# Kernel optimization log

Hardware: AMD Instinct MI355X
Metric: run time of the kernel (lower is better)

The kernel has to match this reference:

```python
import jax, jax.numpy as jnp
import numpy as np

L = 19          # kernel size (module default l=19, odd -> symmetric reflect pad)
PAD = L // 2    # 9


def _sv_blur(x, kernel):
    """Faithful jax version of BatchBlur_SV spatially-varying branch.

    x:      (B, C, H, W) image, C must be 3 (branch hard-codes expand(3,...))
    kernel: (B, H*W, L, L) per-pixel blur kernels
    """
    B, C, H, W = x.shape
    pad = jnp.pad(x, ((0, 0), (0, 0), (PAD, PAD), (PAD, PAD)), mode='reflect')
    # unfold: (B*C, 1, Hp, Wp) -> (B*C, L*L, H, W); channel dim is the L*L taps
    # in row-major (ki, kj) order, matching torch F.unfold for 1-channel input.
    patches = jax.lax.conv_general_dilated_patches(
        pad.reshape(B * C, 1, H + 2 * PAD, W + 2 * PAD),
        filter_shape=(L, L), window_strides=(1, 1), padding='VALID',
        dimension_numbers=('NCHW', 'OIHW', 'NCHW'))
    # -> (B*C, H*W, L*L), batch-major over (b, c) exactly like pad.view(C*B,...)
    patches = patches.reshape(B * C, L * L, H * W).transpose(0, 2, 1)
    # kernel.flatten(2).unsqueeze(0).expand(3,...).view(-1, HW, L*L):
    # channel-major flatten over (c, b) -- reproduce the original ordering.
    kf = jnp.broadcast_to(kernel.reshape(B, H * W, L * L)[None],
                          (C, B, H * W, L * L)).reshape(C * B, H * W, L * L)
    out = jnp.einsum('npk,npk->np', patches, kf)  # multiply + sum over taps
    return out.reshape(B, C, H, W)


def setup_inputs() -> dict:
    key = jax.random.key(0)
    k1, k2 = jax.random.split(key)
    B, C, H, W = 2, 3, 192, 192
    x = jax.random.normal(k1, (B, C, H, W), dtype=jnp.float32)
    kernel = jax.random.uniform(k2, (B, H * W, L, L), dtype=jnp.float32)
    return {"input": x, "kernel": kernel}


def reference(input, kernel):
    return _sv_blur(input, kernel)
```

## Files before the change

### kernel.cpp

```cpp
#include <hip/hip_runtime.h>

#define BB   2
#define CC   3
#define HH   192
#define WW   192
#define LL   19
#define PADR 9
#define HP   (HH + 2 * PADR)
#define WP   (WW + 2 * PADR)
#define HWN  (HH * WW)
#define TAPS (LL * LL)

#define PIXB  16
#define NG16  (HWN / PIXB)
#define TCOLS (PIXB + LL - 1)
#define IF4   (LL * TCOLS)

#define GLOAD_LDS16(g, l)                                                     \
    __builtin_amdgcn_global_load_lds(                                         \
        (const __attribute__((address_space(1))) void*)(g),                   \
        (__attribute__((address_space(3))) void*)(l), 16, 0, 0)

__global__ __launch_bounds__(256) void pad_rearrange(
    const float* __restrict__ x, float4* __restrict__ img) {
    int idx = blockIdx.x * blockDim.x + threadIdx.x;
    const int total = BB * HP * WP;
    if (idx >= total) return;
    int xw  = idx % WP;
    int tmp = idx / WP;
    int y   = tmp % HP;
    int kb  = tmp / HP;
    int oy = y - PADR;
    oy = oy < 0 ? -oy : (oy >= HH ? 2 * HH - 2 - oy : oy);
    int ox = xw - PADR;
    ox = ox < 0 ? -ox : (ox >= WW ? 2 * WW - 2 - ox : ox);
    float v[3];
#pragma unroll
    for (int j = 0; j < 3; ++j) {
        int n = kb + BB * j;
        v[j] = x[((size_t)n * HH + oy) * WW + ox];
    }
    img[idx] = make_float4(v[0], v[1], v[2], 0.0f);
}

__global__ __launch_bounds__(256) void sv_blur16g(
    const float* __restrict__ kern, const float4* __restrict__ img,
    float* __restrict__ out) {
    __shared__ float4 tile[768];

    int bx  = blockIdx.x;
    int kb  = bx / NG16;
    int grp = bx % NG16;
    int p0  = grp * PIXB;
    int h   = p0 / WW, w0 = p0 % WW;
    int tid = threadIdx.x;
    int wv  = tid >> 6;

    const float4* isrc = img + ((size_t)kb * HP + h) * WP + w0;
#pragma unroll
    for (int r = 0; r < 3; ++r) {
        int li = (r << 8) + tid;
        int si = li < IF4 ? li : IF4 - 1;
        int rr = si / TCOLS, cc = si % TCOLS;
        GLOAD_LDS16(isrc + (size_t)rr * WP + cc,
                    (char*)tile + (size_t)(((r << 8) + (wv << 6)) << 4));
    }
    __syncthreads();

    int pp = tid >> 4;
    int q  = tid & 15;
    int p  = p0 + pp;
    const float*  kl = kern + (size_t)(kb * HWN + p) * TAPS + q;
    const float4* tb = tile + pp;

    int kj   = q;
    int ioff = q;
    float a0 = 0.f, a1 = 0.f, a2 = 0.f;
#pragma unroll
    for (int j = 0; j < 22; ++j) {
        float  kv = kl[j << 4];
        float4 iv = tb[ioff];
        a0 = fmaf(kv, iv.x, a0);
        a1 = fmaf(kv, iv.y, a1);
        a2 = fmaf(kv, iv.z, a2);
        bool wrap = kj >= 3;
        ioff += wrap ? 31 : 16;
        kj    = wrap ? kj - 3 : kj + 16;
    }
    {
        if (q < 9) {
            float  kv = kl[22 << 4];
            float4 iv = tb[ioff];
            a0 = fmaf(kv, iv.x, a0);
            a1 = fmaf(kv, iv.y, a1);
            a2 = fmaf(kv, iv.z, a2);
        }
    }
#pragma unroll
    for (int m = 8; m; m >>= 1) {
        a0 += __shfl_xor(a0, m, 64);
        a1 += __shfl_xor(a1, m, 64);
        a2 += __shfl_xor(a2, m, 64);
    }
    if (q < 3) {
        float v = q == 0 ? a0 : (q == 1 ? a1 : a2);
        out[(size_t)(kb + q * BB) * HWN + p] = v;
    }
}

__global__ __launch_bounds__(256) void sv_blur_nows(
    const float* __restrict__ kern, const float* __restrict__ x,
    float* __restrict__ out) {
    int wid  = (blockIdx.x * blockDim.x + threadIdx.x) >> 6;
    int lane = threadIdx.x & 63;
    int p  = wid % HWN;
    int kb = wid / HWN;
    int h = p / WW, w = p % WW;
    const float* kbase = kern + (size_t)(kb * HWN + p) * TAPS;
    float a[3] = {0.f, 0.f, 0.f};
#pragma unroll
    for (int it = 0; it < 6; ++it) {
        int t = lane + 64 * it;
        if (t < TAPS) {
            float kv = kbase[t];
            int ki = t / LL, kj = t % LL;
            int oy = h + ki - PADR;
            oy = oy < 0 ? -oy : (oy >= HH ? 2 * HH - 2 - oy : oy);
            int ox = w + kj - PADR;
            ox = ox < 0 ? -ox : (ox >= WW ? 2 * WW - 2 - ox : ox);
#pragma unroll
            for (int j = 0; j < 3; ++j) {
                int n = kb + BB * j;
                a[j] = fmaf(kv, x[((size_t)n * HH + oy) * WW + ox], a[j]);
            }
        }
    }
#pragma unroll
    for (int m = 32; m; m >>= 1) {
        a[0] += __shfl_xor(a[0], m, 64);
        a[1] += __shfl_xor(a[1], m, 64);
        a[2] += __shfl_xor(a[2], m, 64);
    }
    if (lane == 0) {
#pragma unroll
        for (int j = 0; j < 3; ++j)
            out[(size_t)(kb + j * BB) * HWN + p] = a[j];
    }
}

extern "C" void kernel_launch(void* const* d_in, const int* in_sizes, int n_in,
                              void* d_out, int out_size, void* d_ws, size_t ws_size,
                              hipStream_t stream) {
    const float* x    = (const float*)d_in[0];
    const float* kern = (const float*)d_in[1];
    float*       out  = (float*)d_out;

    const size_t need = (size_t)BB * HP * WP * sizeof(float4);

    if (ws_size >= need) {
        float4* img = (float4*)d_ws;
        const int ptotal = BB * HP * WP;
        pad_rearrange<<<(ptotal + 255) / 256, 256, 0, stream>>>(x, img);
        sv_blur16g<<<BB * NG16, 256, 0, stream>>>(kern, img, out);
    } else {
        const int nwaves  = BB * HWN;
        const int nblocks = nwaves / 4;
        sv_blur_nows<<<nblocks, 256, 0, stream>>>(kern, x, out);
    }
}
```

Measured before the change: 28.04 us.

## Widen blur tile to 32 pixels per block and reduce via DPP row shifts

```diff
diff --git a/kernel.cpp b/kernel.cpp
--- a/kernel.cpp
+++ b/kernel.cpp
@@ -11,8 +11,8 @@
 #define HWN  (HH * WW)
 #define TAPS (LL * LL)
 
-#define PIXB  16
-#define NG16  (HWN / PIXB)
+#define PIXB  32
+#define NG    (HWN / PIXB)
 #define TCOLS (PIXB + LL - 1)
 #define IF4   (LL * TCOLS)
 
@@ -20,6 +20,13 @@
     __builtin_amdgcn_global_load_lds(                                         \
         (const __attribute__((address_space(1))) void*)(g),                   \
         (__attribute__((address_space(3))) void*)(l), 16, 0, 0)
+
+template <int CTRL>
+__device__ __forceinline__ float dpp_add(float a) {
+    int t = __builtin_amdgcn_update_dpp(0, __float_as_int(a), CTRL, 0xf, 0xf,
+                                        true);
+    return a + __int_as_float(t);
+}
 
 __global__ __launch_bounds__(256) void pad_rearrange(
     const float* __restrict__ x, float4* __restrict__ img) {
@@ -43,14 +50,14 @@
     img[idx] = make_float4(v[0], v[1], v[2], 0.0f);
 }
 
-__global__ __launch_bounds__(256) void sv_blur16g(
+__global__ __launch_bounds__(512) void sv_blur32(
     const float* __restrict__ kern, const float4* __restrict__ img,
     float* __restrict__ out) {
-    __shared__ float4 tile[768];
+    __shared__ float4 tile[1024];
 
     int bx  = blockIdx.x;
-    int kb  = bx / NG16;
-    int grp = bx % NG16;
+    int kb  = bx / NG;
+    int grp = bx % NG;
     int p0  = grp * PIXB;
     int h   = p0 / WW, w0 = p0 % WW;
     int tid = threadIdx.x;
@@ -58,12 +65,12 @@
 
     const float4* isrc = img + ((size_t)kb * HP + h) * WP + w0;
 #pragma unroll
-    for (int r = 0; r < 3; ++r) {
-        int li = (r << 8) + tid;
+    for (int r = 0; r < 2; ++r) {
+        int li = (r << 9) + tid;
         int si = li < IF4 ? li : IF4 - 1;
         int rr = si / TCOLS, cc = si % TCOLS;
         GLOAD_LDS16(isrc + (size_t)rr * WP + cc,
-                    (char*)tile + (size_t)(((r << 8) + (wv << 6)) << 4));
+                    (char*)tile + (size_t)(((r << 9) + (wv << 6)) << 4));
     }
     __syncthreads();
 
@@ -84,27 +91,26 @@
         a1 = fmaf(kv, iv.y, a1);
         a2 = fmaf(kv, iv.z, a2);
         bool wrap = kj >= 3;
-        ioff += wrap ? 31 : 16;
+        ioff += wrap ? 47 : 16;
         kj    = wrap ? kj - 3 : kj + 16;
     }
-    {
-        if (q < 9) {
-            float  kv = kl[22 << 4];
-            float4 iv = tb[ioff];
-            a0 = fmaf(kv, iv.x, a0);
-            a1 = fmaf(kv, iv.y, a1);
-            a2 = fmaf(kv, iv.z, a2);
-        }
+    if (q < 9) {
+        float  kv = kl[22 << 4];
+        float4 iv = tb[ioff];
+        a0 = fmaf(kv, iv.x, a0);
+        a1 = fmaf(kv, iv.y, a1);
+        a2 = fmaf(kv, iv.z, a2);
     }
-#pragma unroll
-    for (int m = 8; m; m >>= 1) {
-        a0 += __shfl_xor(a0, m, 64);
-        a1 += __shfl_xor(a1, m, 64);
-        a2 += __shfl_xor(a2, m, 64);
-    }
-    if (q < 3) {
-        float v = q == 0 ? a0 : (q == 1 ? a1 : a2);
-        out[(size_t)(kb + q * BB) * HWN + p] = v;
+
+    a0 = dpp_add<0x111>(a0); a1 = dpp_add<0x111>(a1); a2 = dpp_add<0x111>(a2);
+    a0 = dpp_add<0x112>(a0); a1 = dpp_add<0x112>(a1); a2 = dpp_add<0x112>(a2);
+    a0 = dpp_add<0x114>(a0); a1 = dpp_add<0x114>(a1); a2 = dpp_add<0x114>(a2);
+    a0 = dpp_add<0x118>(a0); a1 = dpp_add<0x118>(a1); a2 = dpp_add<0x118>(a2);
+
+    if (q == 15) {
+        out[(size_t)(kb + 0 * BB) * HWN + p] = a0;
+        out[(size_t)(kb + 1 * BB) * HWN + p] = a1;
+        out[(size_t)(kb + 2 * BB) * HWN + p] = a2;
     }
 }
 
@@ -161,7 +167,7 @@
         float4* img = (float4*)d_ws;
         const int ptotal = BB * HP * WP;
         pad_rearrange<<<(ptotal + 255) / 256, 256, 0, stream>>>(x, img);
-        sv_blur16g<<<BB * NG16, 256, 0, stream>>>(kern, img, out);
+        sv_blur32<<<BB * NG, 512, 0, stream>>>(kern, img, out);
     } else {
         const int nwaves  = BB * HWN;
         const int nblocks = nwaves / 4;
```

After: 28.37 us. No clear change (+1.2%).
